# Kernel tuning notes

Hardware: AMD Instinct MI355X
Metric: run time of the kernel (lower is better)

The kernel has to match this reference:

```python
import jax, jax.numpy as jnp
import numpy as np

FACTOR = 2
GAIN = 1.0

def _setup_fir(fir=(1, 3, 3, 1), gain=GAIN):
    k = np.asarray(fir, dtype=np.float32)
    if k.ndim == 1:
        k = np.outer(k, k)
    k = k / k.sum() * gain
    return k  # (4, 4)

def setup_inputs() -> dict:
    key = jax.random.key(0)
    kx, kw = jax.random.split(key)
    N, C, H, W = 16, 320, 64, 64
    x = jax.random.normal(kx, (N, C, H, W), dtype=jnp.float32)
    # variance-scaling uniform init (DDPM style): fan_in = fan_out = C*9
    fan = C * 3 * 3
    bound = float(np.sqrt(3.0 / fan))
    w = jax.random.uniform(kw, (C, C, 3, 3), dtype=jnp.float32, minval=-bound, maxval=bound)
    fir_k = jnp.asarray(_setup_fir())
    return {"x": x, "w": w, "fir_k": fir_k}

def reference(x, w, fir_k):
    # Fused FIR (upfirdn2d with up=1, down=1) + strided 3x3 conv downsample.
    C = x.shape[1]
    convW = w.shape[3]          # 3
    kH = fir_k.shape[0]         # 4
    p = kH - FACTOR + (convW - 1)           # 4
    pad0, pad1 = (p + 1) // 2, p // 2       # (2, 2)
    # upfirdn2d: zero-pad then true convolution (flipped kernel), depthwise
    xp = jnp.pad(x, ((0, 0), (0, 0), (pad0, pad1), (pad0, pad1)))
    kf = jnp.flip(fir_k, (0, 1))            # symmetric here, kept for faithfulness
    kd = jnp.broadcast_to(kf[None, None], (C, 1, kH, kH))
    y = jax.lax.conv_general_dilated(
        xp, kd, window_strides=(1, 1), padding='VALID',
        dimension_numbers=('NCHW', 'OIHW', 'NCHW'), feature_group_count=C)
    # strided conv2d, padding=0, stride=factor
    out = jax.lax.conv_general_dilated(
        y, w, window_strides=(FACTOR, FACTOR), padding='VALID',
        dimension_numbers=('NCHW', 'OIHW', 'NCHW'))
    return out  # [N, C, H//2, W//2]
```

## Files before the change

kernel.cpp:

```cpp
#include <hip/hip_runtime.h>
#include <hip/hip_bf16.h>


typedef short bf16x8_t __attribute__((ext_vector_type(8)));
typedef float f32x4 __attribute__((ext_vector_type(4)));
typedef unsigned int u32x4 __attribute__((ext_vector_type(4)));
typedef __attribute__((address_space(1))) const unsigned int* as1_u32p;
typedef __attribute__((address_space(3))) unsigned int* as3_u32p;

#define NI 16
#define CCH 320
#define HW 64
#define HY 65
#define HY2 4225
#define CCSTEP 135200

__device__ __forceinline__ float bf16lo(unsigned int u) {
    return __uint_as_float(u << 16);
}
__device__ __forceinline__ float bf16hi(unsigned int u) {
    return __uint_as_float(u & 0xffff0000u);
}

__global__ __launch_bounds__(256) void fir_kernel(const float* __restrict__ x,
                                                  const float* __restrict__ fir_k,
                                                  __hip_bfloat16* __restrict__ yt) {
    __shared__ unsigned short vlds[4 * 8 * 8 * 70];
    int bx = blockIdx.x;
    int n    = bx / 90;
    int rem  = bx % 90;
    int band = rem / 10;
    int cc   = rem % 10;
    int r0   = band * 8;

    float f0 = fir_k[0] + fir_k[1] + fir_k[2] + fir_k[3];
    float f1 = fir_k[4] + fir_k[5] + fir_k[6] + fir_k[7];
    float f2 = fir_k[8] + fir_k[9] + fir_k[10] + fir_k[11];
    float f3 = fir_k[12] + fir_k[13] + fir_k[14] + fir_k[15];

    int tid = threadIdx.x;
    int lane = tid & 63;
    int g = tid >> 6;

    {
        unsigned int* vp = (unsigned int*)(vlds + (size_t)((g * 8 + (lane >> 3)) * 8 + (lane & 7)) * 70);
        vp[0]  = 0;
        vp[33] = 0;
    }

    for (int cp = 0; cp < 4; ++cp) {
        int cisA = cp, cisB = cp + 4;
        const float* xa = x + (size_t)(n * CCH + cc * 32 + g * 8 + cisA) * (HW * HW);
        const float* xc = x + (size_t)(n * CCH + cc * 32 + g * 8 + cisB) * (HW * HW);
        float ra[11], rb[11];
#pragma unroll
        for (int t = 0; t < 11; ++t) {
            int row = r0 + t - 2;
            bool ok = (row >= 0 && row < HW);
            int off = row * HW + lane;
            ra[t] = ok ? xa[off] : 0.f;
            rb[t] = ok ? xc[off] : 0.f;
        }
#pragma unroll
        for (int j = 0; j < 8; ++j) {
            float va = f0 * ra[j] + f1 * ra[j + 1] + f2 * ra[j + 2] + f3 * ra[j + 3];
            float vb = f0 * rb[j] + f1 * rb[j + 1] + f2 * rb[j + 2] + f3 * rb[j + 3];
            vlds[(size_t)((g * 8 + j) * 8 + cisA) * 70 + lane + 2] =
                __bfloat16_as_ushort(__float2bfloat16(va));
            vlds[(size_t)((g * 8 + j) * 8 + cisB) * 70 + lane + 2] =
                __bfloat16_as_ushort(__float2bfloat16(vb));
        }
    }

    asm volatile("s_waitcnt lgkmcnt(0)" ::: "memory");
    __builtin_amdgcn_sched_barrier(0);

    unsigned short* yu = (unsigned short*)yt;
    size_t plane = (size_t)(n * 10 + cc) * HY2;
#pragma unroll
    for (int it = 0; it < 5; ++it) {
        int task = it * 64 + lane;
        if (task < 264) {
            int j  = task / 33;
            int pp = task % 33;
            int c  = 2 * pp;
            int r  = r0 + j;
            if (r < HY) {
                bool pair = (pp < 32);
                float a0[8], a1[8];
#pragma unroll
                for (int k = 0; k < 8; ++k) {
                    const unsigned int* vp = (const unsigned int*)(vlds + (size_t)((g * 8 + j) * 8 + k) * 70 + c);
                    unsigned int u0 = vp[0], u1 = vp[1];
                    float v0 = bf16lo(u0), v1 = bf16hi(u0);
                    float v2 = bf16lo(u1), v3 = bf16hi(u1);
                    a0[k] = f0 * v0 + f1 * v1 + f2 * v2 + f3 * v3;
                    if (pair) {
                        float v4 = bf16lo(vp[2]);
                        a1[k] = f0 * v1 + f1 * v2 + f2 * v3 + f3 * v4;
                    }
                }
                unsigned int w0[4];
#pragma unroll
                for (int h = 0; h < 4; ++h) {
                    unsigned int lo = __bfloat16_as_ushort(__float2bfloat16(a0[2 * h]));
                    unsigned int hi = __bfloat16_as_ushort(__float2bfloat16(a0[2 * h + 1]));
                    w0[h] = lo | (hi << 16);
                }
                size_t base = (plane + (size_t)r * HY + c) * 32 + g * 8;
                *(u32x4*)(yu + base) = (u32x4){w0[0], w0[1], w0[2], w0[3]};
                if (pair) {
                    unsigned int w1[4];
#pragma unroll
                    for (int h = 0; h < 4; ++h) {
                        unsigned int lo = __bfloat16_as_ushort(__float2bfloat16(a1[2 * h]));
                        unsigned int hi = __bfloat16_as_ushort(__float2bfloat16(a1[2 * h + 1]));
                        w1[h] = lo | (hi << 16);
                    }
                    *(u32x4*)(yu + base + 32) = (u32x4){w1[0], w1[1], w1[2], w1[3]};
                }
            }
        }
    }
}

__global__ __launch_bounds__(256) void wt2_kernel(const float* __restrict__ w,
                                                  __hip_bfloat16* __restrict__ wt) {
    int idx = blockIdx.x * 256 + threadIdx.x;
    if (idx < 9 * CCH * CCH) {
        int j  = idx & 7;
        int co = (idx >> 3) % CCH;
        int t2 = idx / 2560;
        int q  = t2 & 3;
        int cc = (t2 >> 2) % 10;
        int tap = t2 / 40;
        int ci = cc * 32 + q * 8 + j;
        wt[idx] = __float2bfloat16(w[(co * CCH + ci) * 9 + tap]);
    }
}

__global__ __launch_bounds__(256, 3) void conv_kernel(const __hip_bfloat16* __restrict__ yt,
                                                      const __hip_bfloat16* __restrict__ wt2,
                                                      float* __restrict__ out) {
    __shared__ short ylds[2][1536 * 8];

    int bx = blockIdx.x;
    int sp = bx & 15;
    int t  = bx >> 4;
    int cb = t % 5;
    int n  = t / 5;
    int co0 = cb * 64;
    int oh0 = (sp >> 1) * 4;
    int ow0 = (sp & 1) * 16;

    int tid = threadIdx.x;
    int lane = tid & 63;
    int wid = tid >> 6;
    int q = lane >> 4, lc = lane & 15;

    const unsigned short* ytu = (const unsigned short*)yt;
    const unsigned short* wtu = (const unsigned short*)wt2;

    int ybase = (n * 10 * HY2 + (2 * oh0) * HY + 2 * ow0) * 32;
    int goff[6];
#pragma unroll
    for (int k = 0; k < 6; ++k) {
        int u = k * 256 + tid;
        int uc = (u < 1485) ? u : 1484;
        int p = uc / 5, s = uc - p * 5;
        if (s == 4) s = 3;
        int pr = p / 33, pc = p - pr * 33;
        goff[k] = ybase + (pr * HY + pc) * 32 + s * 8;
    }

    const unsigned short* wbl = wtu + q * 2560 + (size_t)(co0 + wid * 16 + lc) * 8;
    const int aoff = (2 * lc) * 40 + q * 8;

    f32x4 acc[4];
#pragma unroll
    for (int i = 0; i < 4; ++i) acc[i] = (f32x4){0.f, 0.f, 0.f, 0.f};

    bf16x8_t bfr[2][9];

#define GLDS(buf, K, ccidx)                                                            \
    __builtin_amdgcn_global_load_lds(                                                  \
        (as1_u32p)(ytu + goff[K] + (ccidx) * CCSTEP),                                  \
        (as3_u32p)(&ylds[buf][(size_t)((K) * 256 + wid * 64) * 8]), 16, 0, 0)

#pragma unroll
    for (int k = 0; k < 6; ++k) GLDS(0, k, 0);
#pragma unroll
    for (int kk = 0; kk < 9; ++kk)
        bfr[0][kk] = *(const bf16x8_t*)(wbl + kk * 102400);
    __syncthreads();

    auto compute = [&](const short* buf, const bf16x8_t* b) {
#pragma unroll
        for (int kw = 0; kw < 3; ++kw) {
            bf16x8_t af[9];
#pragma unroll
            for (int r = 0; r < 9; ++r)
                af[r] = *(const bf16x8_t*)(buf + aoff + (r * 33 + kw) * 40);
#pragma unroll
            for (int kh = 0; kh < 3; ++kh)
#pragma unroll
                for (int mf = 0; mf < 4; ++mf)
                    acc[mf] = __builtin_amdgcn_mfma_f32_16x16x32_bf16(
                        b[kh * 3 + kw], af[2 * mf + kh], acc[mf], 0, 0, 0);
        }
    };

    for (int tt = 0; tt < 5; ++tt) {
        int cc0 = 2 * tt, cc1 = 2 * tt + 1;
        {
#pragma unroll
            for (int k = 0; k < 6; ++k) GLDS(1, k, cc0 + 1);
            const unsigned short* wnx = wbl + (cc0 + 1) * 10240;
#pragma unroll
            for (int kk = 0; kk < 9; ++kk)
                bfr[1][kk] = *(const bf16x8_t*)(wnx + kk * 102400);
            compute(&ylds[0][0], bfr[0]);
            __syncthreads();
        }
        {
            if (cc1 < 9) {
#pragma unroll
                for (int k = 0; k < 6; ++k) GLDS(0, k, cc1 + 1);
                const unsigned short* wnx = wbl + (cc1 + 1) * 10240;
#pragma unroll
                for (int kk = 0; kk < 9; ++kk)
                    bfr[0][kk] = *(const bf16x8_t*)(wnx + kk * 102400);
            }
            compute(&ylds[1][0], bfr[1]);
            if (cc1 < 9) __syncthreads();
        }
    }
#undef GLDS

#pragma unroll
    for (int mf = 0; mf < 4; ++mf) {
        int oh = oh0 + mf;
        int ow = ow0 + lc;
#pragma unroll
        for (int rg = 0; rg < 4; ++rg) {
            int co = co0 + wid * 16 + q * 4 + rg;
            out[((n * CCH + co) * 32 + oh) * 32 + ow] = acc[mf][rg];
        }
    }
}

__global__ __launch_bounds__(256) void naive_kernel(const float* __restrict__ x,
                                                    const float* __restrict__ w,
                                                    const float* __restrict__ fk,
                                                    float* __restrict__ out) {
    int idx = blockIdx.x * 256 + threadIdx.x;
    if (idx >= NI * CCH * 32 * 32) return;
    int ow = idx & 31;
    int oh = (idx >> 5) & 31;
    int co = (idx >> 10) % CCH;
    int n = (idx >> 10) / CCH;
    float f0 = fk[0] + fk[1] + fk[2] + fk[3];
    float f1 = fk[4] + fk[5] + fk[6] + fk[7];
    float f2 = fk[8] + fk[9] + fk[10] + fk[11];
    float f3 = fk[12] + fk[13] + fk[14] + fk[15];
    float fv[4] = {f0, f1, f2, f3};
    float acc = 0.f;
    for (int ci = 0; ci < CCH; ++ci) {
        const float* xb = x + (size_t)(n * CCH + ci) * HW * HW;
        const float* wb = w + (size_t)(co * CCH + ci) * 9;
#pragma unroll
        for (int u = 0; u < 3; ++u) {
            int yr = 2 * oh + u;
#pragma unroll
            for (int v = 0; v < 3; ++v) {
                int yc = 2 * ow + v;
                float s = 0.f;
#pragma unroll
                for (int a = 0; a < 4; ++a) {
                    int xrw = yr - 2 + a;
                    if (xrw < 0 || xrw >= HW) continue;
                    float t = 0.f;
#pragma unroll
                    for (int b = 0; b < 4; ++b) {
                        int xc = yc - 2 + b;
                        if (xc >= 0 && xc < HW) t += fv[b] * xb[xrw * HW + xc];
                    }
                    s += fv[a] * t;
                }
                acc += wb[u * 3 + v] * s;
            }
        }
    }
    out[idx] = acc;
}

extern "C" void kernel_launch(void* const* d_in, const int* in_sizes, int n_in,
                              void* d_out, int out_size, void* d_ws, size_t ws_size,
                              hipStream_t stream) {
    const float* x = (const float*)d_in[0];
    const float* w = (const float*)d_in[1];
    const float* fk = (const float*)d_in[2];
    float* out = (float*)d_out;

    const size_t ybytes = (size_t)NI * 10 * HY2 * 32 * 2;
    const size_t wtoff = ybytes;
    const size_t need = wtoff + (size_t)9 * CCH * CCH * 2;

    if (ws_size >= need) {
        __hip_bfloat16* yt = (__hip_bfloat16*)d_ws;
        __hip_bfloat16* wt = (__hip_bfloat16*)((char*)d_ws + wtoff);
        wt2_kernel<<<(9 * CCH * CCH + 255) / 256, 256, 0, stream>>>(w, wt);
        fir_kernel<<<16 * 9 * 10, 256, 0, stream>>>(x, fk, yt);
        conv_kernel<<<16 * 5 * 16, 256, 0, stream>>>(yt, wt, out);
    } else {
        naive_kernel<<<(NI * CCH * 32 * 32 + 255) / 256, 256, 0, stream>>>(x, w, fk, out);
    }
}
```

Baseline: 78.62 us.

## Stage FIR input rows into LDS via async global_load_lds with finer block tiling

The FIR kernel now copies a 7-row by 16-channel input tile straight into LDS with global_load_lds instead of per-thread strided global loads into registers. It zeroes the out-of-range halo rows and computes the vertical pass from LDS. Blocks shrink to 4 output rows by 16 channels, so the grid grows from 1440 to 5440 blocks. The aim is better load coalescing, fewer registers and more parallelism, at the cost of 7/4 vertical halo reloading instead of 11/8. The FIR launch is also moved ahead of the weight transpose.

New measurement: 79.94 us. Within noise of the previous version (+1.7%).

```diff
diff --git a/kernel.cpp b/kernel.cpp
--- a/kernel.cpp
+++ b/kernel.cpp
@@ -25,13 +25,15 @@
 __global__ __launch_bounds__(256) void fir_kernel(const float* __restrict__ x,
                                                   const float* __restrict__ fir_k,
                                                   __hip_bfloat16* __restrict__ yt) {
-    __shared__ unsigned short vlds[4 * 8 * 8 * 70];
+    __shared__ float xls[7 * 16 * 64];
+    __shared__ unsigned short vlds[4 * 16 * 70];
+
     int bx = blockIdx.x;
-    int n    = bx / 90;
-    int rem  = bx % 90;
-    int band = rem / 10;
-    int cc   = rem % 10;
-    int r0   = band * 8;
+    int n    = bx / 340;
+    int rem  = bx % 340;
+    int band = rem / 20;
+    int cig  = rem % 20;
+    int r0   = band * 4;
 
     float f0 = fir_k[0] + fir_k[1] + fir_k[2] + fir_k[3];
     float f1 = fir_k[4] + fir_k[5] + fir_k[6] + fir_k[7];
@@ -42,47 +44,62 @@
     int lane = tid & 63;
     int g = tid >> 6;
 
+    const unsigned int* xb = (const unsigned int*)(x + (size_t)(n * CCH + cig * 16) * (HW * HW));
+#pragma unroll
+    for (int k = 0; k < 7; ++k) {
+        int l16 = k * 256 + tid;
+        int t   = l16 >> 8;
+        int rm  = l16 & 255;
+        int ci  = rm >> 4;
+        int w4  = (rm & 15) * 4;
+        int xrow = r0 + t - 2;
+        int xr = xrow < 0 ? 0 : (xrow > 63 ? 63 : xrow);
+        __builtin_amdgcn_global_load_lds(
+            (as1_u32p)(xb + (size_t)ci * 4096 + xr * 64 + w4),
+            (as3_u32p)((unsigned int*)xls + (size_t)l16 * 4), 16, 0, 0);
+    }
+    __syncthreads();
+
     {
-        unsigned int* vp = (unsigned int*)(vlds + (size_t)((g * 8 + (lane >> 3)) * 8 + (lane & 7)) * 70);
-        vp[0]  = 0;
-        vp[33] = 0;
-    }
-
-    for (int cp = 0; cp < 4; ++cp) {
-        int cisA = cp, cisB = cp + 4;
-        const float* xa = x + (size_t)(n * CCH + cc * 32 + g * 8 + cisA) * (HW * HW);
-        const float* xc = x + (size_t)(n * CCH + cc * 32 + g * 8 + cisB) * (HW * HW);
-        float ra[11], rb[11];
-#pragma unroll
-        for (int t = 0; t < 11; ++t) {
-            int row = r0 + t - 2;
-            bool ok = (row >= 0 && row < HW);
-            int off = row * HW + lane;
-            ra[t] = ok ? xa[off] : 0.f;
-            rb[t] = ok ? xc[off] : 0.f;
-        }
-#pragma unroll
-        for (int j = 0; j < 8; ++j) {
-            float va = f0 * ra[j] + f1 * ra[j + 1] + f2 * ra[j + 2] + f3 * ra[j + 3];
-            float vb = f0 * rb[j] + f1 * rb[j + 1] + f2 * rb[j + 2] + f3 * rb[j + 3];
-            vlds[(size_t)((g * 8 + j) * 8 + cisA) * 70 + lane + 2] =
-                __bfloat16_as_ushort(__float2bfloat16(va));
-            vlds[(size_t)((g * 8 + j) * 8 + cisB) * 70 + lane + 2] =
-                __bfloat16_as_ushort(__float2bfloat16(vb));
-        }
-    }
-
-    asm volatile("s_waitcnt lgkmcnt(0)" ::: "memory");
-    __builtin_amdgcn_sched_barrier(0);
+        int t_lo = 2 - r0;  if (t_lo < 0) t_lo = 0;
+        int t_hi = 66 - r0; if (t_hi > 7) t_hi = 7;
+        if (t_lo > 0 || t_hi < 7) {
+            f32x4 z = (f32x4){0.f, 0.f, 0.f, 0.f};
+            for (int t = 0; t < t_lo; ++t)
+                ((f32x4*)(xls + t * 1024))[tid] = z;
+            for (int t = t_hi; t < 7; ++t)
+                ((f32x4*)(xls + t * 1024))[tid] = z;
+            __syncthreads();
+        }
+    }
+
+#pragma unroll
+    for (int m = 0; m < 16; ++m) {
+        int j   = m >> 2;
+        int cis = g * 4 + (m & 3);
+        int base = cis * 64 + lane;
+        float v = f0 * xls[j * 1024 + base] + f1 * xls[(j + 1) * 1024 + base]
+                + f2 * xls[(j + 2) * 1024 + base] + f3 * xls[(j + 3) * 1024 + base];
+        vlds[(j * 16 + cis) * 70 + lane + 2] = __bfloat16_as_ushort(__float2bfloat16(v));
+    }
+    if (g == 0) {
+        unsigned int* vp = (unsigned int*)vlds + (size_t)lane * 35;
+        vp[0] = 0; vp[33] = 0;
+    }
+    __syncthreads();
 
     unsigned short* yu = (unsigned short*)yt;
+    int cc = cig >> 1;
+    int O  = (cig & 1) * 2;
     size_t plane = (size_t)(n * 10 + cc) * HY2;
 #pragma unroll
-    for (int it = 0; it < 5; ++it) {
-        int task = it * 64 + lane;
+    for (int it = 0; it < 2; ++it) {
+        int task = it * 256 + tid;
         if (task < 264) {
-            int j  = task / 33;
-            int pp = task % 33;
+            int s  = task & 1;
+            int t2 = task >> 1;
+            int j  = t2 / 33;
+            int pp = t2 % 33;
             int c  = 2 * pp;
             int r  = r0 + j;
             if (r < HY) {
@@ -90,7 +107,8 @@
                 float a0[8], a1[8];
 #pragma unroll
                 for (int k = 0; k < 8; ++k) {
-                    const unsigned int* vp = (const unsigned int*)(vlds + (size_t)((g * 8 + j) * 8 + k) * 70 + c);
+                    const unsigned int* vp =
+                        (const unsigned int*)(vlds + (size_t)(j * 16 + s * 8 + k) * 70 + c);
                     unsigned int u0 = vp[0], u1 = vp[1];
                     float v0 = bf16lo(u0), v1 = bf16hi(u0);
                     float v2 = bf16lo(u1), v3 = bf16hi(u1);
@@ -107,7 +125,7 @@
                     unsigned int hi = __bfloat16_as_ushort(__float2bfloat16(a0[2 * h + 1]));
                     w0[h] = lo | (hi << 16);
                 }
-                size_t base = (plane + (size_t)r * HY + c) * 32 + g * 8;
+                size_t base = (plane + (size_t)r * HY + c) * 32 + (O + s) * 8;
                 *(u32x4*)(yu + base) = (u32x4){w0[0], w0[1], w0[2], w0[3]};
                 if (pair) {
                     unsigned int w1[4];
@@ -309,8 +327,8 @@
     if (ws_size >= need) {
         __hip_bfloat16* yt = (__hip_bfloat16*)d_ws;
         __hip_bfloat16* wt = (__hip_bfloat16*)((char*)d_ws + wtoff);
+        fir_kernel<<<16 * 17 * 20, 256, 0, stream>>>(x, fk, yt);
         wt2_kernel<<<(9 * CCH * CCH + 255) / 256, 256, 0, stream>>>(w, wt);
-        fir_kernel<<<16 * 9 * 10, 256, 0, stream>>>(x, fk, yt);
         conv_kernel<<<16 * 5 * 16, 256, 0, stream>>>(yt, wt, out);
     } else {
         naive_kernel<<<(NI * CCH * 32 * 32 + 255) / 256, 256, 0, stream>>>(x, w, fk, out);
```
